# Optimization experiments

Measured on AMD Instinct MI355X. Metric: run time of the kernel, lower is better.

## Reference

```python
import jax, jax.numpy as jnp
import numpy as np

B, T, FS, FC, H, L = 512, 512, 64, 32, 256, 2
LN_EPS = 1e-5


def setup_inputs() -> dict:
    key = jax.random.key(0)
    ks = jax.random.split(key, 16)
    d = {}
    d['seq_features'] = jax.random.normal(ks[0], (B, T, FS), jnp.float32)
    d['context_features'] = jax.random.normal(ks[1], (B, FC), jnp.float32)
    in_sizes = [FS + FC, H]
    i = 2
    for l in range(L):
        fin = in_sizes[l]
        d[f'tau{l}'] = jax.random.normal(ks[i], (H,), jnp.float32) * 0.1; i += 1
        d[f'Win{l}'] = jax.random.normal(ks[i], (H, fin), jnp.float32) * (0.5 / np.sqrt(fin)); i += 1
        d[f'Wrec{l}'] = jax.random.normal(ks[i], (H, H), jnp.float32) * (0.5 / np.sqrt(H)); i += 1
        d[f'Wg{l}'] = jax.random.normal(ks[i], (H, fin + H), jnp.float32) * (0.5 / np.sqrt(fin + H)); i += 1
        d[f'bg{l}'] = jnp.zeros((H,), jnp.float32)
        d[f'lng{l}'] = jnp.ones((H,), jnp.float32)
        d[f'lnb{l}'] = jnp.zeros((H,), jnp.float32)
    d['cW1'] = jax.random.normal(ks[i], (H // 2, H), jnp.float32) / np.sqrt(H); i += 1
    d['cb1'] = jnp.zeros((H // 2,), jnp.float32)
    d['cW2'] = jax.random.normal(ks[i], (1, H // 2), jnp.float32) / np.sqrt(H // 2); i += 1
    d['cb2'] = jnp.zeros((1,), jnp.float32)
    return d


def _cell(x, h, tau, Win, Wrec, Wg, bg, lng, lnb):
    # LTC cell: RK4 integration of dh/dt = -h/tau + W_in x + sigmoid(tanh(gate)) * W_rec h
    taup = jax.nn.softplus(tau) + 1.0  # [H]

    def deriv(hh):
        g = jax.nn.sigmoid(jnp.tanh(jnp.concatenate([x, hh], -1) @ Wg.T + bg))
        return -hh / taup + x @ Win.T + g * (hh @ Wrec.T)

    k1 = deriv(h)
    k2 = deriv(h + 0.5 * k1)
    k3 = deriv(h + 0.5 * k2)
    k4 = deriv(h + k3)
    hn = h + (k1 + 2.0 * k2 + 2.0 * k3 + k4) / 6.0
    mu = jnp.mean(hn, -1, keepdims=True)
    var = jnp.var(hn, -1, keepdims=True)
    hn = (hn - mu) / jnp.sqrt(var + LN_EPS) * lng + lnb
    # torch code clamps to [-10,10] after tanh (no-op numerically, kept for fidelity)
    return jnp.clip(jnp.tanh(hn), -10.0, 10.0)


def reference(seq_features, context_features,
              tau0, Win0, Wrec0, Wg0, bg0, lng0, lnb0,
              tau1, Win1, Wrec1, Wg1, bg1, lng1, lnb1,
              cW1, cb1, cW2, cb2):
    b, t, _ = seq_features.shape
    ctx = jnp.broadcast_to(context_features[:, None, :], (b, t, context_features.shape[-1]))
    x = jnp.concatenate([seq_features, ctx], -1)  # [B, T, FS+FC]
    params = [(tau0, Win0, Wrec0, Wg0, bg0, lng0, lnb0),
              (tau1, Win1, Wrec1, Wg1, bg1, lng1, lnb1)]
    h0 = tuple(jnp.zeros((b, H), x.dtype) for _ in range(L))

    def step(hs, xt):
        inp = xt
        new = []
        for l in range(L):
            hl = _cell(inp, hs[l], *params[l])
            new.append(hl)
            inp = hl
        return tuple(new), None

    hs, _ = jax.lax.scan(step, h0, jnp.swapaxes(x, 0, 1))  # scan over time
    hlast = hs[-1]  # [B, H]
    hid = jax.nn.relu(hlast @ cW1.T + cb1)
    out = hid @ cW2.T + cb2  # [B, 1]
    return out.squeeze(-1)  # [B]
```

## Files before the change

### kernel.cpp

```cpp
#include <hip/hip_runtime.h>
#include <hip/hip_bf16.h>

#define T_  512
#define FS_ 64
#define FC_ 32
#define H_  256
#define APAD 272

#define WS_REC0 0
#define WS_REC1 131072
#define WS_X1P  262144
#define WS_X0S  393216
#define WS_X0C  425984
#define WS_MBOX 458752
#define WS_FLAG_BYTE ((458752 + 262144) * 2)

typedef __attribute__((ext_vector_type(8))) short bfrag;
typedef __attribute__((ext_vector_type(4))) float ffrag;

__device__ __forceinline__ ffrag mfma16(bfrag a, bfrag b, ffrag c) {
    return __builtin_amdgcn_mfma_f32_16x16x32_bf16(a, b, c, 0, 0, 0);
}
__device__ __forceinline__ float fast_tanh(float x) {
    float e = __builtin_amdgcn_exp2f(x * 2.8853901817f);
    return 1.f - 2.f * __builtin_amdgcn_rcpf(e + 1.f);
}
__device__ __forceinline__ void bar_lds() {
    asm volatile("s_waitcnt lgkmcnt(0)\n\ts_barrier" ::: "memory");
}

__global__ __launch_bounds__(256) void prepack_kernel(
    const float* __restrict__ Win0, const float* __restrict__ Wrec0, const float* __restrict__ Wg0,
    const float* __restrict__ Win1, const float* __restrict__ Wrec1, const float* __restrict__ Wg1,
    __hip_bfloat16* __restrict__ ws)
{
    int g = blockIdx.x * 256 + threadIdx.x;
    if (g < 128) ((int*)((char*)ws + WS_FLAG_BYTE))[g] = 0;
    if (g >= 55296) return;
    int lane = g & 63;
    int frag = g >> 6;
    int lm = lane & 15, qq = lane >> 4;
    const float* src;
    int dstoff;
    if (frag < 256) {
        int f = frag, ft = f >> 3, ks = f & 7;
        int n = (ft >> 1) * 16 + lm, kk = ks * 32 + qq * 8;
        src = (ft & 1) ? (Wrec0 + n * 256 + kk) : (Wg0 + n * 352 + 96 + kk);
        dstoff = WS_REC0 + (f * 64 + lane) * 8;
    } else if (frag < 512) {
        int f = frag - 256, ft = f >> 3, ks = f & 7;
        int n = (ft >> 1) * 16 + lm, kk = ks * 32 + qq * 8;
        src = (ft & 1) ? (Wrec1 + n * 256 + kk) : (Wg1 + n * 512 + 256 + kk);
        dstoff = WS_REC1 + (f * 64 + lane) * 8;
    } else if (frag < 768) {
        int f = frag - 512, ft = f >> 3, ks = f & 7;
        int n = (ft >> 1) * 16 + lm, kk = ks * 32 + qq * 8;
        src = (ft & 1) ? (Wg1 + n * 512 + kk) : (Win1 + n * 256 + kk);
        dstoff = WS_X1P + (f * 64 + lane) * 8;
    } else if (frag < 832) {
        int f = frag - 768, ft = f >> 1, ks = f & 1;
        int n = (ft >> 1) * 16 + lm, kk = ks * 32 + qq * 8;
        src = (ft & 1) ? (Wg0 + n * 352 + kk) : (Win0 + n * 96 + kk);
        dstoff = WS_X0S + (f * 64 + lane) * 8;
    } else {
        int f = frag - 832, ft = f;
        int n = (ft >> 1) * 16 + lm, kk = qq * 8;
        src = (ft & 1) ? (Wg0 + n * 352 + 64 + kk) : (Win0 + n * 96 + 64 + kk);
        dstoff = WS_X0C + (f * 64 + lane) * 8;
    }
    __hip_bfloat16* d = ws + dstoff;
#pragma unroll
    for (int j = 0; j < 8; j++) d[j] = __float2bfloat16(src[j]);
}

__global__ __launch_bounds__(512, 2) void lnn_main(
    const float* __restrict__ seq, const float* __restrict__ ctx,
    const float* __restrict__ tau0, const float* __restrict__ bg0,
    const float* __restrict__ lng0, const float* __restrict__ lnb0,
    const float* __restrict__ tau1, const float* __restrict__ bg1,
    const float* __restrict__ lng1, const float* __restrict__ lnb1,
    const float* __restrict__ cW1, const float* __restrict__ cb1,
    const float* __restrict__ cW2, const float* __restrict__ cb2,
    __hip_bfloat16* __restrict__ ws, float* __restrict__ out)
{
    __shared__ __align__(16) float hbuf[16][260];
    __shared__ __align__(16) float hn[16][260];
    __shared__ __align__(16) __hip_bfloat16 abf[2][16][APAD];
    __shared__ __align__(16) __hip_bfloat16 x1A[16][APAD];
    __shared__ __align__(16) __hip_bfloat16 xsb[16][80];
    __shared__ __align__(16) float lnw[256], lnb[256];

    const int tid  = threadIdx.x;
    const int wave = tid >> 6, lane = tid & 63;
    const int qq   = lane >> 4, lm = lane & 15;
    const int bid  = blockIdx.x;
    const int tile = bid & 31, roleB = bid >> 5;
    const int brow = tile * 16;

    int* flags = (int*)((char*)ws + WS_FLAG_BYTE);
    int* pubf  = flags + tile * 2;
    int* ackf  = flags + 64 + tile * 2;
    __hip_bfloat16* mb0 = ws + WS_MBOX + tile * 2 * 4096;

    for (int e = tid; e < 16 * 260; e += 512) ((float*)hbuf)[e] = 0.f;
    for (int e = tid; e < 2 * 16 * APAD; e += 512)
        ((__hip_bfloat16*)abf)[e] = __float2bfloat16(0.f);
    if (tid < 256) {
        const float* lg = roleB ? lng1 : lng0;
        const float* lb = roleB ? lnb1 : lnb0;
        lnw[tid] = lg[tid]; lnb[tid] = lb[tid];
    }
    float rtp[2], bgr[2];
#pragma unroll
    for (int b = 0; b < 2; b++) {
        int colb = wave * 32 + b * 16 + lm;
        float tv = roleB ? tau1[colb] : tau0[colb];
        float sp = fmaxf(tv, 0.f) + logf(1.f + __expf(-fabsf(tv)));
        rtp[b] = 1.f / (sp + 1.f);
        bgr[b] = roleB ? bg1[colb] : bg0[colb];
    }

    bfrag cg[2][8], cr[2][8];
    {
        const __hip_bfloat16* rp = ws + (roleB ? WS_REC1 : WS_REC0);
#pragma unroll
        for (int b = 0; b < 2; b++) {
            int ct = 2 * wave + b;
#pragma unroll
            for (int ks = 0; ks < 8; ks++) {
                cg[b][ks] = *(const bfrag*)(rp + ((16 * ct + ks) * 64 + lane) * 8);
                cr[b][ks] = *(const bfrag*)(rp + ((16 * ct + 8 + ks) * 64 + lane) * 8);
            }
        }
    }

    float xwin[2][4], xgate[2][4], hbase[2][4], hh[2][4], ksum[2][4];

    auto deriv = [&](const __hip_bfloat16 (*Ar)[APAD], __hip_bfloat16 (*Aw)[APAD], int d) {
        ffrag ag[2], ar[2];
#pragma unroll
        for (int b = 0; b < 2; b++) {
            ag[b] = (ffrag){0.f, 0.f, 0.f, 0.f};
            ar[b] = (ffrag){0.f, 0.f, 0.f, 0.f};
        }
#pragma unroll
        for (int ks = 0; ks < 8; ks++) {
            bfrag a = *(const bfrag*)&Ar[lm][ks * 32 + qq * 8];
            ag[0] = mfma16(a, cg[0][ks], ag[0]);
            ar[0] = mfma16(a, cr[0][ks], ar[0]);
            ag[1] = mfma16(a, cg[1][ks], ag[1]);
            ar[1] = mfma16(a, cr[1][ks], ar[1]);
        }
        float wsm = (d == 1 || d == 2) ? 2.f : 1.f;
        float an  = (d < 2) ? 0.5f : 1.f;
#pragma unroll
        for (int b = 0; b < 2; b++) {
            int colb = wave * 32 + b * 16 + lm;
#pragma unroll
            for (int r = 0; r < 4; r++) {
                float t  = fast_tanh(ag[b][r] + xgate[b][r]);
                float t2 = t * t;
                float g  = 0.5f + t * (0.25f + t2 * (-(1.f / 48.f) + t2 * (1.f / 480.f)));
                float kd = xwin[b][r] - hh[b][r] * rtp[b] + g * ar[b][r];
                ksum[b][r] += wsm * kd;
                if (d < 3) {
                    float hhn = hbase[b][r] + an * kd;
                    hh[b][r] = hhn;
                    Aw[qq * 4 + r][colb] = __float2bfloat16(hhn);
                } else {
                    hn[qq * 4 + r][colb] = hbase[b][r] + ksum[b][r] * (1.f / 6.f);
                }
            }
        }
    };
    auto loadbase = [&]() {
#pragma unroll
        for (int b = 0; b < 2; b++) {
            int colb = wave * 32 + b * 16 + lm;
#pragma unroll
            for (int r = 0; r < 4; r++) {
                float v = hbuf[qq * 4 + r][colb];
                hbase[b][r] = v; hh[b][r] = v; ksum[b][r] = 0.f;
            }
        }
    };
    auto lnorm = [&](__hip_bfloat16* mbslot) {
#pragma unroll
        for (int i = 0; i < 2; i++) {
            int rr = wave + i * 8, c0 = lane * 4;
            float4 vv = *(const float4*)&hn[rr][c0];
            float v[4] = {vv.x, vv.y, vv.z, vv.w};
            float s  = v[0] + v[1] + v[2] + v[3];
            float s2 = v[0]*v[0] + v[1]*v[1] + v[2]*v[2] + v[3]*v[3];
#pragma unroll
            for (int m = 1; m <= 32; m <<= 1) {
                s  += __shfl_xor(s, m, 64);
                s2 += __shfl_xor(s2, m, 64);
            }
            float mean = s * (1.f / 256.f);
            float var  = s2 * (1.f / 256.f) - mean * mean;
            float rs   = __builtin_amdgcn_rsqf(var + 1e-5f);
            float4 lw = *(const float4*)&lnw[c0];
            float4 lb = *(const float4*)&lnb[c0];
            float hv[4];
            __align__(8) __hip_bfloat16 hb[4];
            hv[0] = fast_tanh((v[0] - mean) * rs * lw.x + lb.x);
            hv[1] = fast_tanh((v[1] - mean) * rs * lw.y + lb.y);
            hv[2] = fast_tanh((v[2] - mean) * rs * lw.z + lb.z);
            hv[3] = fast_tanh((v[3] - mean) * rs * lw.w + lb.w);
#pragma unroll
            for (int j = 0; j < 4; j++) hb[j] = __float2bfloat16(hv[j]);
            *(float4*)&hbuf[rr][c0] = (float4){hv[0], hv[1], hv[2], hv[3]};
            *(uint2*)&abf[0][rr][c0] = *(uint2*)hb;
            if (mbslot)
                __hip_atomic_store((unsigned long long*)&mbslot[rr * 256 + c0],
                                   *(unsigned long long*)hb,
                                   __ATOMIC_RELAXED, __HIP_MEMORY_SCOPE_AGENT);
        }
    };

    if (!roleB) {
        for (int e = tid; e < 16 * FC_; e += 512) {
            int r = e >> 5, c = e & 31;
            xsb[r][c] = __float2bfloat16(ctx[(brow + r) * FC_ + c]);
        }
        __syncthreads();
        float xcw[2][4], xcg[2][4];
#pragma unroll
        for (int b = 0; b < 2; b++) {
            int ct = 2 * wave + b;
            bfrag a = *(const bfrag*)&xsb[lm][qq * 8];
            ffrag zw = {0.f, 0.f, 0.f, 0.f}, zg = {0.f, 0.f, 0.f, 0.f};
            bfrag bw  = *(const bfrag*)(ws + WS_X0C + ((2 * ct) * 64 + lane) * 8);
            bfrag bgf = *(const bfrag*)(ws + WS_X0C + ((2 * ct + 1) * 64 + lane) * 8);
            zw = mfma16(a, bw, zw);
            zg = mfma16(a, bgf, zg);
#pragma unroll
            for (int r = 0; r < 4; r++) { xcw[b][r] = zw[r]; xcg[b][r] = zg[r]; }
        }
        __syncthreads();
        float seqv0 = seq[((size_t)(brow + wave) * T_ + 0) * FS_ + lane];
        float seqv1 = seq[((size_t)(brow + wave + 8) * T_ + 0) * FS_ + lane];

#pragma unroll 1
        for (int t = 0; t < T_; t++) {
            int p = t & 1;
            const __hip_bfloat16* x0s = ws + WS_X0S;
            asm volatile("" : "+s"(x0s));

            xsb[wave][lane]     = __float2bfloat16(seqv0);
            xsb[wave + 8][lane] = __float2bfloat16(seqv1);
            if (tid == 0 && t >= 2) {
                int guard = 1 << 27;
                while (__hip_atomic_load(&ackf[p], __ATOMIC_RELAXED,
                                         __HIP_MEMORY_SCOPE_AGENT) < t - 1 && --guard) {}
            }
            __syncthreads();
            {
                bfrag a0 = *(const bfrag*)&xsb[lm][qq * 8];
                bfrag a1 = *(const bfrag*)&xsb[lm][32 + qq * 8];
#pragma unroll
                for (int b = 0; b < 2; b++) {
                    int ct = 2 * wave + b;
                    bfrag w0 = *(const bfrag*)(x0s + ((4 * ct + 0) * 64 + lane) * 8);
                    bfrag w1 = *(const bfrag*)(x0s + ((4 * ct + 1) * 64 + lane) * 8);
                    bfrag g0 = *(const bfrag*)(x0s + ((4 * ct + 2) * 64 + lane) * 8);
                    bfrag g1 = *(const bfrag*)(x0s + ((4 * ct + 3) * 64 + lane) * 8);
                    ffrag zw, zg;
#pragma unroll
                    for (int r = 0; r < 4; r++) { zw[r] = xcw[b][r]; zg[r] = xcg[b][r] + bgr[b]; }
                    zw = mfma16(a0, w0, zw); zw = mfma16(a1, w1, zw);
                    zg = mfma16(a0, g0, zg); zg = mfma16(a1, g1, zg);
#pragma unroll
                    for (int r = 0; r < 4; r++) { xwin[b][r] = zw[r]; xgate[b][r] = zg[r]; }
                }
                loadbase();
                int tn = (t + 1 < T_) ? t + 1 : t;
                seqv0 = seq[((size_t)(brow + wave) * T_ + tn) * FS_ + lane];
                seqv1 = seq[((size_t)(brow + wave + 8) * T_ + tn) * FS_ + lane];
                deriv(abf[0], abf[1], 0);
            }
            bar_lds(); deriv(abf[1], abf[0], 1);
            bar_lds(); deriv(abf[0], abf[1], 2);
            bar_lds(); deriv(abf[1], abf[0], 3);
            bar_lds();
            lnorm(mb0 + p * 4096);
            asm volatile("s_waitcnt vmcnt(0)" ::: "memory");
            __syncthreads();
            if (tid == 0)
                __hip_atomic_store(&pubf[p], t + 1, __ATOMIC_RELEASE,
                                   __HIP_MEMORY_SCOPE_AGENT);
        }
        return;
    }

#pragma unroll 1
    for (int t = 0; t < T_; t++) {
        int p = t & 1;
        const __hip_bfloat16* xp = ws + WS_X1P;
        asm volatile("" : "+s"(xp));
        if (tid == 0) {
            int guard = 1 << 27;
            while (__hip_atomic_load(&pubf[p], __ATOMIC_RELAXED,
                                     __HIP_MEMORY_SCOPE_AGENT) < t + 1 && --guard) {}
        }
        __syncthreads();
        {
            int r = tid >> 5, c0 = (tid & 31) * 8;
            unsigned long long v0 = __hip_atomic_load(
                (const unsigned long long*)&mb0[p * 4096 + r * 256 + c0],
                __ATOMIC_RELAXED, __HIP_MEMORY_SCOPE_AGENT);
            unsigned long long v1 = __hip_atomic_load(
                (const unsigned long long*)&mb0[p * 4096 + r * 256 + c0 + 4],
                __ATOMIC_RELAXED, __HIP_MEMORY_SCOPE_AGENT);
            *(unsigned long long*)&x1A[r][c0]     = v0;
            *(unsigned long long*)&x1A[r][c0 + 4] = v1;
        }
        __syncthreads();
        if (tid == 0)
            __hip_atomic_store(&ackf[p], t + 1, __ATOMIC_RELEASE,
                               __HIP_MEMORY_SCOPE_AGENT);
        {
            ffrag zw[2], zg[2];
#pragma unroll
            for (int b = 0; b < 2; b++) {
                zw[b] = (ffrag){0.f, 0.f, 0.f, 0.f};
#pragma unroll
                for (int r = 0; r < 4; r++) zg[b][r] = bgr[b];
            }
#pragma unroll
            for (int b = 0; b < 2; b++) {
                int ct = 2 * wave + b;
#pragma unroll
                for (int half = 0; half < 2; half++) {
                    bfrag wv[4], gv[4];
#pragma unroll
                    for (int j = 0; j < 4; j++) {
                        int ks = half * 4 + j;
                        wv[j] = *(const bfrag*)(xp + ((16 * ct + ks) * 64 + lane) * 8);
                        gv[j] = *(const bfrag*)(xp + ((16 * ct + 8 + ks) * 64 + lane) * 8);
                    }
#pragma unroll
                    for (int j = 0; j < 4; j++) {
                        int ks = half * 4 + j;
                        bfrag a = *(const bfrag*)&x1A[lm][ks * 32 + qq * 8];
                        zw[b] = mfma16(a, wv[j], zw[b]);
                        zg[b] = mfma16(a, gv[j], zg[b]);
                    }
                }
            }
#pragma unroll
            for (int b = 0; b < 2; b++)
#pragma unroll
                for (int r = 0; r < 4; r++) { xwin[b][r] = zw[b][r]; xgate[b][r] = zg[b][r]; }
            loadbase();
            deriv(abf[0], abf[1], 0);
        }
        bar_lds(); deriv(abf[1], abf[0], 1);
        bar_lds(); deriv(abf[0], abf[1], 2);
        bar_lds(); deriv(abf[1], abf[0], 3);
        bar_lds();
        lnorm(nullptr);
        __syncthreads();
    }

#pragma unroll
    for (int i = 0; i < 2; i++) {
        int rr = wave + i * 8;
        float acc0 = cb1[lane], acc1 = cb1[lane + 64];
        const float* w0 = cW1 + (size_t)lane * H_;
        const float* w1 = cW1 + (size_t)(lane + 64) * H_;
        for (int k = 0; k < H_; k += 4) {
            float4 hv = *(const float4*)&hbuf[rr][k];
            acc0 += hv.x * w0[k] + hv.y * w0[k+1] + hv.z * w0[k+2] + hv.w * w0[k+3];
            acc1 += hv.x * w1[k] + hv.y * w1[k+1] + hv.z * w1[k+2] + hv.w * w1[k+3];
        }
        __syncthreads();
        hn[rr][lane]      = fmaxf(acc0, 0.f);
        hn[rr][lane + 64] = fmaxf(acc1, 0.f);
    }
    __syncthreads();
    if (tid < 16) {
        float acc = cb2[0];
        for (int k = 0; k < 128; k++) acc += hn[tid][k] * cW2[k];
        out[brow + tid] = acc;
    }
}

extern "C" void kernel_launch(void* const* d_in, const int* in_sizes, int n_in,
                              void* d_out, int out_size, void* d_ws, size_t ws_size,
                              hipStream_t stream) {
    const float* seq   = (const float*)d_in[0];
    const float* ctx   = (const float*)d_in[1];
    const float* tau0  = (const float*)d_in[2];
    const float* Win0  = (const float*)d_in[3];
    const float* Wrec0 = (const float*)d_in[4];
    const float* Wg0   = (const float*)d_in[5];
    const float* bg0   = (const float*)d_in[6];
    const float* lng0  = (const float*)d_in[7];
    const float* lnb0  = (const float*)d_in[8];
    const float* tau1  = (const float*)d_in[9];
    const float* Win1  = (const float*)d_in[10];
    const float* Wrec1 = (const float*)d_in[11];
    const float* Wg1   = (const float*)d_in[12];
    const float* bg1   = (const float*)d_in[13];
    const float* lng1  = (const float*)d_in[14];
    const float* lnb1  = (const float*)d_in[15];
    const float* cW1   = (const float*)d_in[16];
    const float* cb1   = (const float*)d_in[17];
    const float* cW2   = (const float*)d_in[18];
    const float* cb2   = (const float*)d_in[19];
    __hip_bfloat16* ws = (__hip_bfloat16*)d_ws;

    hipLaunchKernelGGL(prepack_kernel, dim3(216), dim3(256), 0, stream,
                       Win0, Wrec0, Wg0, Win1, Wrec1, Wg1, ws);
    hipLaunchKernelGGL(lnn_main, dim3(64), dim3(512), 0, stream,
                       seq, ctx, tau0, bg0, lng0, lnb0, tau1, bg1, lng1, lnb1,
                       cW1, cb1, cW2, cb2, ws, (float*)d_out);
}
```

Baseline: 4.441 ms.

## Swap MFMA operands, drop per-step barriers and LDS staging in recurrent loop

```diff
diff --git a/kernel.cpp b/kernel.cpp
--- a/kernel.cpp
+++ b/kernel.cpp
@@ -17,6 +17,7 @@
 
 typedef __attribute__((ext_vector_type(8))) short bfrag;
 typedef __attribute__((ext_vector_type(4))) float ffrag;
+typedef __attribute__((ext_vector_type(4))) float f32x4;
 
 __device__ __forceinline__ ffrag mfma16(bfrag a, bfrag b, ffrag c) {
     return __builtin_amdgcn_mfma_f32_16x16x32_bf16(a, b, c, 0, 0, 0);
@@ -86,8 +87,7 @@
     __shared__ __align__(16) float hbuf[16][260];
     __shared__ __align__(16) float hn[16][260];
     __shared__ __align__(16) __hip_bfloat16 abf[2][16][APAD];
-    __shared__ __align__(16) __hip_bfloat16 x1A[16][APAD];
-    __shared__ __align__(16) __hip_bfloat16 xsb[16][80];
+    __shared__ __align__(16) __hip_bfloat16 xsb[16][40];
     __shared__ __align__(16) float lnw[256], lnb[256];
 
     const int tid  = threadIdx.x;
@@ -110,15 +110,17 @@
         const float* lb = roleB ? lnb1 : lnb0;
         lnw[tid] = lg[tid]; lnb[tid] = lb[tid];
     }
-    float rtp[2], bgr[2];
-#pragma unroll
-    for (int b = 0; b < 2; b++) {
-        int colb = wave * 32 + b * 16 + lm;
-        float tv = roleB ? tau1[colb] : tau0[colb];
-        float sp = fmaxf(tv, 0.f) + logf(1.f + __expf(-fabsf(tv)));
-        rtp[b] = 1.f / (sp + 1.f);
-        bgr[b] = roleB ? bg1[colb] : bg0[colb];
-    }
+    float rtp_t[2][4], bgr_t[2][4];
+#pragma unroll
+    for (int b = 0; b < 2; b++)
+#pragma unroll
+        for (int r = 0; r < 4; r++) {
+            int n = wave * 32 + b * 16 + qq * 4 + r;
+            float tv = roleB ? tau1[n] : tau0[n];
+            float sp = fmaxf(tv, 0.f) + logf(1.f + __expf(-fabsf(tv)));
+            rtp_t[b][r] = 1.f / (sp + 1.f);
+            bgr_t[b][r] = roleB ? bg1[n] : bg0[n];
+        }
 
     bfrag cg[2][8], cr[2][8];
     {
@@ -133,6 +135,15 @@
             }
         }
     }
+    auto pinrec = [&]() {
+#pragma unroll
+        for (int b = 0; b < 2; b++)
+#pragma unroll
+            for (int ks = 0; ks < 8; ks++) {
+                asm volatile("" : "+v"(cg[b][ks]));
+                asm volatile("" : "+v"(cr[b][ks]));
+            }
+    };
 
     float xwin[2][4], xgate[2][4], hbase[2][4], hh[2][4], ksum[2][4];
 
@@ -146,50 +157,67 @@
 #pragma unroll
         for (int ks = 0; ks < 8; ks++) {
             bfrag a = *(const bfrag*)&Ar[lm][ks * 32 + qq * 8];
-            ag[0] = mfma16(a, cg[0][ks], ag[0]);
-            ar[0] = mfma16(a, cr[0][ks], ar[0]);
-            ag[1] = mfma16(a, cg[1][ks], ag[1]);
-            ar[1] = mfma16(a, cr[1][ks], ar[1]);
+            ag[0] = mfma16(cg[0][ks], a, ag[0]);
+            ar[0] = mfma16(cr[0][ks], a, ar[0]);
+            ag[1] = mfma16(cg[1][ks], a, ag[1]);
+            ar[1] = mfma16(cr[1][ks], a, ar[1]);
         }
         float wsm = (d == 1 || d == 2) ? 2.f : 1.f;
         float an  = (d < 2) ? 0.5f : 1.f;
 #pragma unroll
         for (int b = 0; b < 2; b++) {
-            int colb = wave * 32 + b * 16 + lm;
-#pragma unroll
-            for (int r = 0; r < 4; r++) {
-                float t  = fast_tanh(ag[b][r] + xgate[b][r]);
-                float t2 = t * t;
-                float g  = 0.5f + t * (0.25f + t2 * (-(1.f / 48.f) + t2 * (1.f / 480.f)));
-                float kd = xwin[b][r] - hh[b][r] * rtp[b] + g * ar[b][r];
-                ksum[b][r] += wsm * kd;
-                if (d < 3) {
+            int n0b = wave * 32 + b * 16 + qq * 4;
+            if (d < 3) {
+                __align__(8) __hip_bfloat16 hb[4];
+#pragma unroll
+                for (int r = 0; r < 4; r++) {
+                    float t  = fast_tanh(ag[b][r] + xgate[b][r]);
+                    float t2 = t * t;
+                    float g  = 0.5f + t * (0.25f + t2 * (-(1.f / 48.f) + t2 * (1.f / 480.f)));
+                    float kd = xwin[b][r] - hh[b][r] * rtp_t[b][r] + g * ar[b][r];
+                    ksum[b][r] += wsm * kd;
                     float hhn = hbase[b][r] + an * kd;
                     hh[b][r] = hhn;
-                    Aw[qq * 4 + r][colb] = __float2bfloat16(hhn);
-                } else {
-                    hn[qq * 4 + r][colb] = hbase[b][r] + ksum[b][r] * (1.f / 6.f);
+                    hb[r] = __float2bfloat16(hhn);
                 }
+                *(uint2*)&Aw[lm][n0b] = *(uint2*)hb;
+            } else {
+                f32x4 o;
+#pragma unroll
+                for (int r = 0; r < 4; r++) {
+                    float t  = fast_tanh(ag[b][r] + xgate[b][r]);
+                    float t2 = t * t;
+                    float g  = 0.5f + t * (0.25f + t2 * (-(1.f / 48.f) + t2 * (1.f / 480.f)));
+                    float kd = xwin[b][r] - hh[b][r] * rtp_t[b][r] + g * ar[b][r];
+                    ksum[b][r] += kd;
+                    o[r] = hbase[b][r] + ksum[b][r] * (1.f / 6.f);
+                }
+                *(f32x4*)&hn[lm][n0b] = o;
             }
         }
     };
     auto loadbase = [&]() {
 #pragma unroll
         for (int b = 0; b < 2; b++) {
-            int colb = wave * 32 + b * 16 + lm;
+            int n0b = wave * 32 + b * 16 + qq * 4;
+            f32x4 v = *(const f32x4*)&hbuf[lm][n0b];
 #pragma unroll
             for (int r = 0; r < 4; r++) {
-                float v = hbuf[qq * 4 + r][colb];
-                hbase[b][r] = v; hh[b][r] = v; ksum[b][r] = 0.f;
+                hbase[b][r] = v[r]; hh[b][r] = v[r]; ksum[b][r] = 0.f;
             }
         }
     };
-    auto lnorm = [&](__hip_bfloat16* mbslot) {
+    auto lnorm = [&](__hip_bfloat16* mbslot, int t) {
+        if (mbslot && t >= 2) {
+            int p = t & 1, guard = 1 << 27;
+            while (__hip_atomic_load(&ackf[p], __ATOMIC_RELAXED,
+                                     __HIP_MEMORY_SCOPE_AGENT) < t - 1 && --guard) {}
+        }
 #pragma unroll
         for (int i = 0; i < 2; i++) {
             int rr = wave + i * 8, c0 = lane * 4;
-            float4 vv = *(const float4*)&hn[rr][c0];
-            float v[4] = {vv.x, vv.y, vv.z, vv.w};
+            f32x4 vv = *(const f32x4*)&hn[rr][c0];
+            float v[4] = {vv[0], vv[1], vv[2], vv[3]};
             float s  = v[0] + v[1] + v[2] + v[3];
             float s2 = v[0]*v[0] + v[1]*v[1] + v[2]*v[2] + v[3]*v[3];
 #pragma unroll
@@ -200,17 +228,16 @@
             float mean = s * (1.f / 256.f);
             float var  = s2 * (1.f / 256.f) - mean * mean;
             float rs   = __builtin_amdgcn_rsqf(var + 1e-5f);
-            float4 lw = *(const float4*)&lnw[c0];
-            float4 lb = *(const float4*)&lnb[c0];
+            f32x4 lw = *(const f32x4*)&lnw[c0];
+            f32x4 lb = *(const f32x4*)&lnb[c0];
             float hv[4];
             __align__(8) __hip_bfloat16 hb[4];
-            hv[0] = fast_tanh((v[0] - mean) * rs * lw.x + lb.x);
-            hv[1] = fast_tanh((v[1] - mean) * rs * lw.y + lb.y);
-            hv[2] = fast_tanh((v[2] - mean) * rs * lw.z + lb.z);
-            hv[3] = fast_tanh((v[3] - mean) * rs * lw.w + lb.w);
-#pragma unroll
-            for (int j = 0; j < 4; j++) hb[j] = __float2bfloat16(hv[j]);
-            *(float4*)&hbuf[rr][c0] = (float4){hv[0], hv[1], hv[2], hv[3]};
+#pragma unroll
+            for (int j = 0; j < 4; j++) {
+                hv[j] = fast_tanh((v[j] - mean) * rs * lw[j] + lb[j]);
+                hb[j] = __float2bfloat16(hv[j]);
+            }
+            *(f32x4*)&hbuf[rr][c0] = (f32x4){hv[0], hv[1], hv[2], hv[3]};
             *(uint2*)&abf[0][rr][c0] = *(uint2*)hb;
             if (mbslot)
                 __hip_atomic_store((unsigned long long*)&mbslot[rr * 256 + c0],
@@ -233,58 +260,63 @@
             ffrag zw = {0.f, 0.f, 0.f, 0.f}, zg = {0.f, 0.f, 0.f, 0.f};
             bfrag bw  = *(const bfrag*)(ws + WS_X0C + ((2 * ct) * 64 + lane) * 8);
             bfrag bgf = *(const bfrag*)(ws + WS_X0C + ((2 * ct + 1) * 64 + lane) * 8);
-            zw = mfma16(a, bw, zw);
-            zg = mfma16(a, bgf, zg);
+            zw = mfma16(bw, a, zw);
+            zg = mfma16(bgf, a, zg);
 #pragma unroll
             for (int r = 0; r < 4; r++) { xcw[b][r] = zw[r]; xcg[b][r] = zg[r]; }
         }
         __syncthreads();
-        float seqv0 = seq[((size_t)(brow + wave) * T_ + 0) * FS_ + lane];
-        float seqv1 = seq[((size_t)(brow + wave + 8) * T_ + 0) * FS_ + lane];
+
+        const float* sq0 = seq + ((size_t)(brow + lm) * T_) * FS_ + qq * 8;
+        f32x4 sf0 = *(const f32x4*)(sq0);
+        f32x4 sf1 = *(const f32x4*)(sq0 + 4);
+        f32x4 sf2 = *(const f32x4*)(sq0 + 32);
+        f32x4 sf3 = *(const f32x4*)(sq0 + 36);
 
 #pragma unroll 1
         for (int t = 0; t < T_; t++) {
             int p = t & 1;
+            pinrec();
             const __hip_bfloat16* x0s = ws + WS_X0S;
             asm volatile("" : "+s"(x0s));
-
-            xsb[wave][lane]     = __float2bfloat16(seqv0);
-            xsb[wave + 8][lane] = __float2bfloat16(seqv1);
-            if (tid == 0 && t >= 2) {
-                int guard = 1 << 27;
-                while (__hip_atomic_load(&ackf[p], __ATOMIC_RELAXED,
-                                         __HIP_MEMORY_SCOPE_AGENT) < t - 1 && --guard) {}
-            }
-            __syncthreads();
+            union { bfrag v; __hip_bfloat16 h[8]; } ua0, ua1;
+#pragma unroll
+            for (int j = 0; j < 4; j++) {
+                ua0.h[j]     = __float2bfloat16(sf0[j]);
+                ua0.h[j + 4] = __float2bfloat16(sf1[j]);
+                ua1.h[j]     = __float2bfloat16(sf2[j]);
+                ua1.h[j + 4] = __float2bfloat16(sf3[j]);
+            }
             {
-                bfrag a0 = *(const bfrag*)&xsb[lm][qq * 8];
-                bfrag a1 = *(const bfrag*)&xsb[lm][32 + qq * 8];
-#pragma unroll
-                for (int b = 0; b < 2; b++) {
-                    int ct = 2 * wave + b;
-                    bfrag w0 = *(const bfrag*)(x0s + ((4 * ct + 0) * 64 + lane) * 8);
-                    bfrag w1 = *(const bfrag*)(x0s + ((4 * ct + 1) * 64 + lane) * 8);
-                    bfrag g0 = *(const bfrag*)(x0s + ((4 * ct + 2) * 64 + lane) * 8);
-                    bfrag g1 = *(const bfrag*)(x0s + ((4 * ct + 3) * 64 + lane) * 8);
-                    ffrag zw, zg;
-#pragma unroll
-                    for (int r = 0; r < 4; r++) { zw[r] = xcw[b][r]; zg[r] = xcg[b][r] + bgr[b]; }
-                    zw = mfma16(a0, w0, zw); zw = mfma16(a1, w1, zw);
-                    zg = mfma16(a0, g0, zg); zg = mfma16(a1, g1, zg);
-#pragma unroll
-                    for (int r = 0; r < 4; r++) { xwin[b][r] = zw[r]; xgate[b][r] = zg[r]; }
-                }
-                loadbase();
                 int tn = (t + 1 < T_) ? t + 1 : t;
-                seqv0 = seq[((size_t)(brow + wave) * T_ + tn) * FS_ + lane];
-                seqv1 = seq[((size_t)(brow + wave + 8) * T_ + tn) * FS_ + lane];
-                deriv(abf[0], abf[1], 0);
-            }
+                const float* sp = seq + ((size_t)(brow + lm) * T_ + tn) * FS_ + qq * 8;
+                sf0 = *(const f32x4*)(sp);
+                sf1 = *(const f32x4*)(sp + 4);
+                sf2 = *(const f32x4*)(sp + 32);
+                sf3 = *(const f32x4*)(sp + 36);
+            }
+#pragma unroll
+            for (int b = 0; b < 2; b++) {
+                int ct = 2 * wave + b;
+                bfrag w0 = *(const bfrag*)(x0s + ((4 * ct + 0) * 64 + lane) * 8);
+                bfrag w1 = *(const bfrag*)(x0s + ((4 * ct + 1) * 64 + lane) * 8);
+                bfrag g0 = *(const bfrag*)(x0s + ((4 * ct + 2) * 64 + lane) * 8);
+                bfrag g1 = *(const bfrag*)(x0s + ((4 * ct + 3) * 64 + lane) * 8);
+                ffrag zw, zg;
+#pragma unroll
+                for (int r = 0; r < 4; r++) { zw[r] = xcw[b][r]; zg[r] = xcg[b][r] + bgr_t[b][r]; }
+                zw = mfma16(w0, ua0.v, zw); zw = mfma16(w1, ua1.v, zw);
+                zg = mfma16(g0, ua0.v, zg); zg = mfma16(g1, ua1.v, zg);
+#pragma unroll
+                for (int r = 0; r < 4; r++) { xwin[b][r] = zw[r]; xgate[b][r] = zg[r]; }
+            }
+            loadbase();
+            deriv(abf[0], abf[1], 0);
             bar_lds(); deriv(abf[1], abf[0], 1);
             bar_lds(); deriv(abf[0], abf[1], 2);
             bar_lds(); deriv(abf[1], abf[0], 3);
             bar_lds();
-            lnorm(mb0 + p * 4096);
+            lnorm(mb0 + p * 4096, t);
             asm volatile("s_waitcnt vmcnt(0)" ::: "memory");
             __syncthreads();
             if (tid == 0)
@@ -297,40 +329,31 @@
 #pragma unroll 1
     for (int t = 0; t < T_; t++) {
         int p = t & 1;
+        pinrec();
         const __hip_bfloat16* xp = ws + WS_X1P;
         asm volatile("" : "+s"(xp));
-        if (tid == 0) {
+        {
             int guard = 1 << 27;
             while (__hip_atomic_load(&pubf[p], __ATOMIC_RELAXED,
                                      __HIP_MEMORY_SCOPE_AGENT) < t + 1 && --guard) {}
         }
-        __syncthreads();
+        bfrag am[8];
+#pragma unroll
+        for (int ks = 0; ks < 8; ks++) {
+            const unsigned long long* q =
+                (const unsigned long long*)(mb0 + p * 4096 + lm * 256 + ks * 32 + qq * 8);
+            union { unsigned long long u[2]; bfrag v; } x;
+            x.u[0] = __hip_atomic_load(q,     __ATOMIC_RELAXED, __HIP_MEMORY_SCOPE_AGENT);
+            x.u[1] = __hip_atomic_load(q + 1, __ATOMIC_RELAXED, __HIP_MEMORY_SCOPE_AGENT);
+            am[ks] = x.v;
+        }
         {
-            int r = tid >> 5, c0 = (tid & 31) * 8;
-            unsigned long long v0 = __hip_atomic_load(
-                (const unsigned long long*)&mb0[p * 4096 + r * 256 + c0],
-                __ATOMIC_RELAXED, __HIP_MEMORY_SCOPE_AGENT);
-            unsigned long long v1 = __hip_atomic_load(
-                (const unsigned long long*)&mb0[p * 4096 + r * 256 + c0 + 4],
-                __ATOMIC_RELAXED, __HIP_MEMORY_SCOPE_AGENT);
-            *(unsigned long long*)&x1A[r][c0]     = v0;
-            *(unsigned long long*)&x1A[r][c0 + 4] = v1;
-        }
-        __syncthreads();
-        if (tid == 0)
-            __hip_atomic_store(&ackf[p], t + 1, __ATOMIC_RELEASE,
-                               __HIP_MEMORY_SCOPE_AGENT);
-        {
-            ffrag zw[2], zg[2];
-#pragma unroll
-            for (int b = 0; b < 2; b++) {
-                zw[b] = (ffrag){0.f, 0.f, 0.f, 0.f};
-#pragma unroll
-                for (int r = 0; r < 4; r++) zg[b][r] = bgr[b];
-            }
 #pragma unroll
             for (int b = 0; b < 2; b++) {
                 int ct = 2 * wave + b;
+                ffrag zw, zg;
+#pragma unroll
+                for (int r = 0; r < 4; r++) { zw[r] = 0.f; zg[r] = bgr_t[b][r]; }
 #pragma unroll
                 for (int half = 0; half < 2; half++) {
                     bfrag wv[4], gv[4];
@@ -343,24 +366,25 @@
 #pragma unroll
                     for (int j = 0; j < 4; j++) {
                         int ks = half * 4 + j;
-                        bfrag a = *(const bfrag*)&x1A[lm][ks * 32 + qq * 8];
-                        zw[b] = mfma16(a, wv[j], zw[b]);
-                        zg[b] = mfma16(a, gv[j], zg[b]);
+                        zw = mfma16(wv[j], am[ks], zw);
+                        zg = mfma16(gv[j], am[ks], zg);
                     }
                 }
-            }
-#pragma unroll
-            for (int b = 0; b < 2; b++)
-#pragma unroll
-                for (int r = 0; r < 4; r++) { xwin[b][r] = zw[b][r]; xgate[b][r] = zg[b][r]; }
-            loadbase();
-            deriv(abf[0], abf[1], 0);
-        }
-        bar_lds(); deriv(abf[1], abf[0], 1);
+#pragma unroll
+                for (int r = 0; r < 4; r++) { xwin[b][r] = zw[r]; xgate[b][r] = zg[r]; }
+            }
+        }
+        loadbase();
+        deriv(abf[0], abf[1], 0);
+        bar_lds();
+        if (tid == 0)
+            __hip_atomic_store(&ackf[p], t + 1, __ATOMIC_RELEASE,
+                               __HIP_MEMORY_SCOPE_AGENT);
+        deriv(abf[1], abf[0], 1);
         bar_lds(); deriv(abf[0], abf[1], 2);
         bar_lds(); deriv(abf[1], abf[0], 3);
         bar_lds();
-        lnorm(nullptr);
+        lnorm(nullptr, t);
         __syncthreads();
     }
 
@@ -371,9 +395,9 @@
         const float* w0 = cW1 + (size_t)lane * H_;
         const float* w1 = cW1 + (size_t)(lane + 64) * H_;
         for (int k = 0; k < H_; k += 4) {
-            float4 hv = *(const float4*)&hbuf[rr][k];
-            acc0 += hv.x * w0[k] + hv.y * w0[k+1] + hv.z * w0[k+2] + hv.w * w0[k+3];
-            acc1 += hv.x * w1[k] + hv.y * w1[k+1] + hv.z * w1[k+2] + hv.w * w1[k+3];
+            f32x4 hv = *(const f32x4*)&hbuf[rr][k];
+            acc0 += hv[0] * w0[k] + hv[1] * w0[k+1] + hv[2] * w0[k+2] + hv[3] * w0[k+3];
+            acc1 += hv[0] * w1[k] + hv[1] * w1[k+1] + hv[2] * w1[k+2] + hv[3] * w1[k+3];
         }
         __syncthreads();
         hn[rr][lane]      = fmaxf(acc0, 0.f);
```

Result: slower. 6.008 ms (+35.3%).
